# Kernel optimization log

Hardware: AMD Instinct MI355X
Metric: run time of the kernel (lower is better)

## Reference

```python
import jax, jax.numpy as jnp
import numpy as np
from functools import partial

L, B, E, H, NL = 512, 16, 768, 12, 12
D = E // H  # head dim = 64
FF = 4 * E
LN_EPS = 1e-5


def gelu_new(x):
    # HF openai-gpt ACT_FNS['gelu'] (tanh approximation)
    c = np.sqrt(2.0 / np.pi).astype(np.float32)
    return 0.5 * x * (1.0 + jnp.tanh(c * (x + 0.044715 * x * x * x)))


def layer_norm(x, g, b):
    mu = jnp.mean(x, axis=-1, keepdims=True)
    var = jnp.mean(jnp.square(x - mu), axis=-1, keepdims=True)
    return (x - mu) * jax.lax.rsqrt(var + LN_EPS) * g + b


def setup_inputs() -> dict:
    key = jax.random.key(0)
    ks = jax.random.split(key, 8)
    s = 0.02
    x = jax.random.normal(ks[0], (L, B, E), dtype=jnp.float32)
    custom_mask = jnp.ones((B, L), dtype=jnp.float32)
    pos_emb = s * jax.random.normal(ks[1], (L, E), dtype=jnp.float32)
    # stacked per-layer params (leading axis = layer)
    params = {
        'c_attn_w': s * jax.random.normal(ks[2], (NL, E, 3 * E), dtype=jnp.float32),
        'c_attn_b': jnp.zeros((NL, 3 * E), dtype=jnp.float32),
        'attn_proj_w': s * jax.random.normal(ks[3], (NL, E, E), dtype=jnp.float32),
        'attn_proj_b': jnp.zeros((NL, E), dtype=jnp.float32),
        'ln1_g': jnp.ones((NL, E), dtype=jnp.float32),
        'ln1_b': jnp.zeros((NL, E), dtype=jnp.float32),
        'c_fc_w': s * jax.random.normal(ks[4], (NL, E, FF), dtype=jnp.float32),
        'c_fc_b': jnp.zeros((NL, FF), dtype=jnp.float32),
        'mlp_proj_w': s * jax.random.normal(ks[5], (NL, FF, E), dtype=jnp.float32),
        'mlp_proj_b': jnp.zeros((NL, E), dtype=jnp.float32),
        'ln2_g': jnp.ones((NL, E), dtype=jnp.float32),
        'ln2_b': jnp.zeros((NL, E), dtype=jnp.float32),
    }
    return {'x': x, 'custom_mask': custom_mask, 'pos_emb': pos_emb, **params}


def _gpt_forward(x, custom_mask, pos_emb, c_attn_w, c_attn_b, attn_proj_w,
                 attn_proj_b, ln1_g, ln1_b, c_fc_w, c_fc_b, mlp_proj_w,
                 mlp_proj_b, ln2_g, ln2_b):
    Lx, Bx, Ex = x.shape
    h = x.transpose(1, 0, 2) + pos_emb[None, :Lx]  # (B, L, E); dropout = eval identity
    # additive padding mask: (1 - m) * finfo.min, broadcast over heads/queries
    add_mask = (1.0 - custom_mask)[:, None, None, :] * jnp.finfo(jnp.float32).min
    causal = jnp.tril(jnp.ones((Lx, Lx), dtype=jnp.float32))  # bias buffer b

    def block(h, p):
        (caw, cab, apw, apb, g1, b1, fw, fb, pw, pb, g2, b2) = p
        qkv = h @ caw + cab                              # (B, L, 3E)
        q, k, v = jnp.split(qkv, 3, axis=-1)
        q = q.reshape(Bx, Lx, H, D).transpose(0, 2, 1, 3)  # (B, H, L, D)
        k = k.reshape(Bx, Lx, H, D).transpose(0, 2, 1, 3)
        v = v.reshape(Bx, Lx, H, D).transpose(0, 2, 1, 3)
        w = jnp.einsum('bhqd,bhkd->bhqk', q, k) / np.float32(np.sqrt(D))
        w = w * causal + (-10000.0) * (1.0 - causal)     # causal bias masking
        w = w + add_mask
        a = jax.nn.softmax(w, axis=-1)
        o = jnp.einsum('bhqk,bhkd->bhqd', a, v)          # (B, H, L, D)
        o = o.transpose(0, 2, 1, 3).reshape(Bx, Lx, Ex)
        a_out = o @ apw + apb
        n = layer_norm(h + a_out, g1, b1)
        m = gelu_new(n @ fw + fb) @ pw + pb
        h2 = layer_norm(n + m, g2, b2)
        return h2, None

    params = (c_attn_w, c_attn_b, attn_proj_w, attn_proj_b, ln1_g, ln1_b,
              c_fc_w, c_fc_b, mlp_proj_w, mlp_proj_b, ln2_g, ln2_b)
    h, _ = jax.lax.scan(block, h, params)
    return h.transpose(1, 0, 2)  # back to (L, B, E)


def reference(x, custom_mask, pos_emb, c_attn_w, c_attn_b, attn_proj_w,
              attn_proj_b, ln1_g, ln1_b, c_fc_w, c_fc_b, mlp_proj_w,
              mlp_proj_b, ln2_g, ln2_b):
    return _gpt_forward(x, custom_mask, pos_emb, c_attn_w, c_attn_b,
                        attn_proj_w, attn_proj_b, ln1_g, ln1_b, c_fc_w,
                        c_fc_b, mlp_proj_w, mlp_proj_b, ln2_g, ln2_b)
```

## Files before the change

### kernel.cpp

```cpp
#include <hip/hip_runtime.h>
#include <cstdint>
#include <cstddef>


#define LSEQ 512
#define NBATCH 16
#define EDIM 768
#define NHEAD 12
#define NLAYER 12

typedef __attribute__((ext_vector_type(8))) short short8;
typedef __attribute__((ext_vector_type(4))) float f32x4;

__device__ __forceinline__ short f2bf(float f) {
  union { float f; unsigned u; } x; x.f = f;
  return (short)((x.u + 0x7FFFu + ((x.u >> 16) & 1u)) >> 16);
}

__device__ __forceinline__ void gload_lds16(const void* g, void* l) {
  __builtin_amdgcn_global_load_lds(
      (__attribute__((address_space(1))) void*)(void*)g,
      (__attribute__((address_space(3))) void*)l, 16, 0, 0);
}

__global__ __launch_bounds__(256) void wt_transpose(const float* __restrict__ W,
                                                    short* __restrict__ Wt,
                                                    int K, int N) {
  __shared__ float tile[32][33];
  const int n0 = blockIdx.x * 32, k0 = blockIdx.y * 32;
  const size_t lo = (size_t)blockIdx.z * K * N;
  const float* Ws = W + lo;
  short* Wd = Wt + lo;
  const int tx = threadIdx.x & 31, ty = threadIdx.x >> 5;
#pragma unroll
  for (int i = 0; i < 4; ++i)
    tile[ty + i * 8][tx] = Ws[(size_t)(k0 + ty + i * 8) * N + n0 + tx];
  __syncthreads();
#pragma unroll
  for (int i = 0; i < 4; ++i)
    Wd[(size_t)(n0 + ty + i * 8) * K + k0 + tx] = f2bf(tile[tx][ty + i * 8]);
}

__global__ __launch_bounds__(256) void embed_k(const float* __restrict__ x,
                                               const float* __restrict__ pos,
                                               float* __restrict__ h,
                                               short* __restrict__ hbf) {
  const int row = blockIdx.x;
  const int b = row >> 9, lp = row & 511;
  const int t = threadIdx.x;
#pragma unroll
  for (int i = 0; i < 3; ++i) {
    const int e = t + i * 256;
    float v = x[(size_t)(lp * 16 + b) * 768 + e] + pos[(size_t)lp * 768 + e];
    h[(size_t)row * 768 + e] = v;
    hbf[(size_t)row * 768 + e] = f2bf(v);
  }
}

__global__ __launch_bounds__(256) void final_k(const float* __restrict__ h,
                                               float* __restrict__ out) {
  const int row = blockIdx.x;
  const int lp = row >> 4, b = row & 15;
  const int t = threadIdx.x;
#pragma unroll
  for (int i = 0; i < 3; ++i) {
    const int e = t + i * 256;
    out[(size_t)row * 768 + e] = h[(size_t)(b * 512 + lp) * 768 + e];
  }
}

__global__ __launch_bounds__(256) void ln_fused(const float* __restrict__ A,
                                                const float* __restrict__ B,
                                                const float* __restrict__ g,
                                                const float* __restrict__ be,
                                                float* __restrict__ outf,
                                                short* __restrict__ outb) {
  const int row = blockIdx.x;
  const int t = threadIdx.x;
  const size_t base = (size_t)row * 768;
  float v[3];
  float s1 = 0.f, s2 = 0.f;
#pragma unroll
  for (int i = 0; i < 3; ++i) {
    const int e = t + i * 256;
    float xv = A[base + e] + B[base + e];
    v[i] = xv; s1 += xv; s2 += xv * xv;
  }
#pragma unroll
  for (int m = 1; m < 64; m <<= 1) {
    s1 += __shfl_xor(s1, m);
    s2 += __shfl_xor(s2, m);
  }
  __shared__ float r1[4], r2[4];
  const int w = t >> 6, l = t & 63;
  if (l == 0) { r1[w] = s1; r2[w] = s2; }
  __syncthreads();
  s1 = r1[0] + r1[1] + r1[2] + r1[3];
  s2 = r2[0] + r2[1] + r2[2] + r2[3];
  const float mu = s1 * (1.f / 768.f);
  const float var = s2 * (1.f / 768.f) - mu * mu;
  const float rs = rsqrtf(var + 1e-5f);
#pragma unroll
  for (int i = 0; i < 3; ++i) {
    const int e = t + i * 256;
    float o = (v[i] - mu) * rs * g[e] + be[e];
    outf[base + e] = o;
    outb[base + e] = f2bf(o);
  }
}

template <int TN, int EPI>
__global__ __launch_bounds__(256) void gemm_bt(const short* __restrict__ A,
                                               const short* __restrict__ Bt,
                                               const float* __restrict__ bias,
                                               void* __restrict__ C,
                                               int N, int K) {
  constexpr int BK = 64;
  __shared__ alignas(16) short Alds[128 * BK];
  __shared__ alignas(16) short Blds[TN * BK];
  const int t = threadIdx.x;
  const int w = t >> 6, l = t & 63;
  constexpr int WR = (TN == 128) ? 2 : 4;
  constexpr int WC = (TN == 128) ? 2 : 1;
  constexpr int WM = 128 / WR;
  constexpr int MI = WM / 16;
  constexpr int NI = (TN / WC) / 16;
  const int wr = (WC == 2) ? (w >> 1) : w;
  const int wc = (WC == 2) ? (w & 1) : 0;
  const int l15 = l & 15, lhi = l >> 4;
  const int rowA0 = blockIdx.x * 128;
  const int rowB0 = blockIdx.y * TN;
  f32x4 acc[MI][NI];
#pragma unroll
  for (int mi = 0; mi < MI; ++mi)
#pragma unroll
    for (int ni = 0; ni < NI; ++ni) acc[mi][ni] = (f32x4){0.f, 0.f, 0.f, 0.f};

  const int srl = l >> 3;
  const int ss = l & 7;

  for (int kt = 0; kt < K; kt += BK) {
#pragma unroll
    for (int i = 0; i < 4; ++i) {
      const int r = i * 32 + w * 8 + srl;
      gload_lds16(A + (size_t)(rowA0 + r) * K + kt + ((ss ^ (r & 7)) << 3),
                  &Alds[i * 2048 + w * 512]);
    }
#pragma unroll
    for (int i = 0; i < TN / 32; ++i) {
      const int r = i * 32 + w * 8 + srl;
      gload_lds16(Bt + (size_t)(rowB0 + r) * K + kt + ((ss ^ (r & 7)) << 3),
                  &Blds[i * 2048 + w * 512]);
    }
    __syncthreads();
    short8 af[MI][2], bfr[NI][2];
#pragma unroll
    for (int mi = 0; mi < MI; ++mi) {
      const int r = wr * WM + mi * 16 + l15;
#pragma unroll
      for (int kc = 0; kc < 2; ++kc)
        af[mi][kc] = *(const short8*)
            &Alds[r * 64 + ((((kc << 2) | lhi) ^ (r & 7)) << 3)];
    }
#pragma unroll
    for (int ni = 0; ni < NI; ++ni) {
      const int r = wc * 64 + ni * 16 + l15;
#pragma unroll
      for (int kc = 0; kc < 2; ++kc)
        bfr[ni][kc] = *(const short8*)
            &Blds[r * 64 + ((((kc << 2) | lhi) ^ (r & 7)) << 3)];
    }
#pragma unroll
    for (int mi = 0; mi < MI; ++mi)
#pragma unroll
      for (int ni = 0; ni < NI; ++ni)
#pragma unroll
        for (int kc = 0; kc < 2; ++kc)
          acc[mi][ni] = __builtin_amdgcn_mfma_f32_16x16x32_bf16(
              af[mi][kc], bfr[ni][kc], acc[mi][ni], 0, 0, 0);
    __syncthreads();
  }

  float bv[NI];
#pragma unroll
  for (int ni = 0; ni < NI; ++ni) bv[ni] = bias[rowB0 + wc * 64 + ni * 16 + l15];
#pragma unroll
  for (int mi = 0; mi < MI; ++mi) {
#pragma unroll
    for (int ni = 0; ni < NI; ++ni) {
      const int col = rowB0 + wc * 64 + ni * 16 + l15;
#pragma unroll
      for (int i = 0; i < 4; ++i) {
        const int row = rowA0 + wr * WM + mi * 16 + lhi * 4 + i;
        float v = acc[mi][ni][i] + bv[ni];
        if constexpr (EPI == 0) {
          ((float*)C)[(size_t)row * N + col] = v;
        } else if constexpr (EPI == 1) {
          ((short*)C)[(size_t)row * N + col] = f2bf(v);
        } else {
          float z = 0.7978845608028654f * (v + 0.044715f * v * v * v);
          float th = 1.0f - 2.0f / (__expf(2.0f * z) + 1.0f);
          ((short*)C)[(size_t)row * N + col] = f2bf(0.5f * v * (1.0f + th));
        }
      }
    }
  }
}

__global__ __launch_bounds__(256) void attn_k(const short* __restrict__ qkv,
                                              const float* __restrict__ mask,
                                              short* __restrict__ o) {
  const int qb = blockIdx.x;
  const int hh = blockIdx.y;
  const int b = blockIdx.z;
  const int t = threadIdx.x, w = t >> 6, l = t & 63;
  const int l15 = l & 15, lhi = l >> 4;
  __shared__ alignas(16) short Klds[64 * 64];
  __shared__ alignas(16) short Vlds[64 * 64];
  __shared__ alignas(16) short Plds[4][16 * 72];

  short8 qa[2];
  {
    const size_t base =
        (size_t)(b * LSEQ + qb * 64 + w * 16 + l15) * 2304 + hh * 64;
    qa[0] = *(const short8*)&qkv[base + lhi * 8];
    qa[1] = *(const short8*)&qkv[base + 32 + lhi * 8];
  }
  float mrow[4] = {-1e30f, -1e30f, -1e30f, -1e30f};
  float lrow[4] = {0.f, 0.f, 0.f, 0.f};
  const f32x4 zero4 = {0.f, 0.f, 0.f, 0.f};
  f32x4 oacc[4];
#pragma unroll
  for (int nt = 0; nt < 4; ++nt) oacc[nt] = zero4;

  const int nkt = qb + 1;
  for (int kt = 0; kt < nkt; ++kt) {
    __syncthreads();
    {
      const int kr = t >> 2, cc = (t & 3) * 16;
      const size_t grow = (size_t)(b * LSEQ + kt * 64 + kr) * 2304 + hh * 64;
      short8 k0 = *(const short8*)&qkv[grow + 768 + cc];
      short8 k1 = *(const short8*)&qkv[grow + 768 + cc + 8];
      short8 v0 = *(const short8*)&qkv[grow + 1536 + cc];
      short8 v1 = *(const short8*)&qkv[grow + 1536 + cc + 8];
      const int sw = (kr & 7) << 4;
      *(short8*)((char*)Klds + ((kr * 128 + cc * 2) ^ sw)) = k0;
      *(short8*)((char*)Klds + ((kr * 128 + cc * 2 + 16) ^ sw)) = k1;
#pragma unroll
      for (int e = 0; e < 8; ++e) {
        const int n0 = cc + e, n1 = cc + 8 + e;
        ((short*)Vlds)[((n0 * 128 + kr * 2) ^ ((n0 & 7) << 4)) >> 1] = v0[e];
        ((short*)Vlds)[((n1 * 128 + kr * 2) ^ ((n1 & 7) << 4)) >> 1] = v1[e];
      }
    }
    __syncthreads();

    f32x4 s[4];
#pragma unroll
    for (int jt = 0; jt < 4; ++jt) {
      f32x4 z = zero4;
#pragma unroll
      for (int kc = 0; kc < 2; ++kc) {
        const int rowk = jt * 16 + l15;
        short8 kb = *(const short8*)((char*)Klds +
                     ((rowk * 128 + kc * 64 + lhi * 16) ^ ((rowk & 7) << 4)));
        z = __builtin_amdgcn_mfma_f32_16x16x32_bf16(qa[kc], kb, z, 0, 0, 0);
      }
      s[jt] = z;
    }

    float addm[4];
#pragma unroll
    for (int jt = 0; jt < 4; ++jt)
      addm[jt] = (1.0f - mask[b * LSEQ + kt * 64 + jt * 16 + l15]) *
                 -3.402823466e38f;
#pragma unroll
    for (int jt = 0; jt < 4; ++jt) {
      const int colg = kt * 64 + jt * 16 + l15;
#pragma unroll
      for (int i = 0; i < 4; ++i) {
        const int rowg = qb * 64 + w * 16 + lhi * 4 + i;
        float sv = s[jt][i] * 0.125f;
        if (colg > rowg) sv = -10000.0f;
        s[jt][i] = sv + addm[jt];
      }
    }

    float mnew[4], sc[4];
#pragma unroll
    for (int i = 0; i < 4; ++i) {
      float tm = fmaxf(fmaxf(s[0][i], s[1][i]), fmaxf(s[2][i], s[3][i]));
#pragma unroll
      for (int mm = 1; mm < 16; mm <<= 1) tm = fmaxf(tm, __shfl_xor(tm, mm));
      mnew[i] = fmaxf(mrow[i], tm);
      sc[i] = __expf(mrow[i] - mnew[i]);
      mrow[i] = mnew[i];
    }
#pragma unroll
    for (int i = 0; i < 4; ++i) {
      float ts = 0.f;
#pragma unroll
      for (int jt = 0; jt < 4; ++jt) {
        float p = __expf(s[jt][i] - mnew[i]);
        s[jt][i] = p;
        ts += p;
      }
#pragma unroll
      for (int mm = 1; mm < 16; mm <<= 1) ts += __shfl_xor(ts, mm);
      lrow[i] = lrow[i] * sc[i] + ts;
      oacc[0][i] *= sc[i]; oacc[1][i] *= sc[i];
      oacc[2][i] *= sc[i]; oacc[3][i] *= sc[i];
    }

    short* Pw = &Plds[w][0];
#pragma unroll
    for (int jt = 0; jt < 4; ++jt)
#pragma unroll
      for (int i = 0; i < 4; ++i)
        Pw[(lhi * 4 + i) * 72 + jt * 16 + l15] = f2bf(s[jt][i]);
    __syncthreads();
    short8 pa[2];
#pragma unroll
    for (int kc = 0; kc < 2; ++kc)
      pa[kc] = *(const short8*)&Pw[l15 * 72 + kc * 32 + lhi * 8];

#pragma unroll
    for (int nt = 0; nt < 4; ++nt) {
#pragma unroll
      for (int kc = 0; kc < 2; ++kc) {
        const int rown = nt * 16 + l15;
        short8 vb = *(const short8*)((char*)Vlds +
                     ((rown * 128 + kc * 64 + lhi * 16) ^ ((rown & 7) << 4)));
        oacc[nt] = __builtin_amdgcn_mfma_f32_16x16x32_bf16(pa[kc], vb,
                                                           oacc[nt], 0, 0, 0);
      }
    }
  }

#pragma unroll
  for (int i = 0; i < 4; ++i) {
    const size_t row = (size_t)(b * LSEQ + qb * 64 + w * 16 + lhi * 4 + i);
    const float inv = 1.0f / lrow[i];
#pragma unroll
    for (int nt = 0; nt < 4; ++nt)
      o[row * 768 + hh * 64 + nt * 16 + l15] = f2bf(oacc[nt][i] * inv);
  }
}

extern "C" void kernel_launch(void* const* d_in, const int* in_sizes, int n_in,
                              void* d_out, int out_size, void* d_ws,
                              size_t ws_size, hipStream_t stream) {
  const float* x    = (const float*)d_in[0];
  const float* mask = (const float*)d_in[1];
  const float* pos  = (const float*)d_in[2];
  const float* caw  = (const float*)d_in[3];
  const float* cab  = (const float*)d_in[4];
  const float* apw  = (const float*)d_in[5];
  const float* apb  = (const float*)d_in[6];
  const float* g1   = (const float*)d_in[7];
  const float* b1   = (const float*)d_in[8];
  const float* fw   = (const float*)d_in[9];
  const float* fb   = (const float*)d_in[10];
  const float* pw   = (const float*)d_in[11];
  const float* pb   = (const float*)d_in[12];
  const float* g2   = (const float*)d_in[13];
  const float* b2   = (const float*)d_in[14];

  char* ws = (char*)d_ws;
  size_t off = 0;
  auto alloc = [&](size_t bytes) {
    size_t o = off;
    off += (bytes + 255) & ~(size_t)255;
    return o;
  };
  float* h    = (float*)(ws + alloc(8192ull * 768 * 4));
  short* hbf  = (short*)(ws + alloc(8192ull * 768 * 2));
  float* nrm  = (float*)(ws + alloc(8192ull * 768 * 4));
  short* nbf  = (short*)(ws + alloc(8192ull * 768 * 2));
  short* qkvb = (short*)(ws + alloc(8192ull * 2304 * 2));
  short* obf  = (short*)(ws + alloc(8192ull * 768 * 2));
  float* aout = (float*)(ws + alloc(8192ull * 768 * 4));
  short* gbf  = (short*)(ws + alloc(8192ull * 3072 * 2));
  short* wt_attn = (short*)(ws + alloc(12ull * 768 * 2304 * 2));
  short* wt_proj = (short*)(ws + alloc(12ull * 768 * 768 * 2));
  short* wt_fc   = (short*)(ws + alloc(12ull * 768 * 3072 * 2));
  short* wt_mlp  = (short*)(ws + alloc(12ull * 3072 * 768 * 2));
  (void)ws_size; (void)in_sizes; (void)n_in; (void)out_size;

  wt_transpose<<<dim3(2304 / 32, 768 / 32, 12), 256, 0, stream>>>(caw, wt_attn, 768, 2304);
  wt_transpose<<<dim3(768 / 32, 768 / 32, 12), 256, 0, stream>>>(apw, wt_proj, 768, 768);
  wt_transpose<<<dim3(3072 / 32, 768 / 32, 12), 256, 0, stream>>>(fw, wt_fc, 768, 3072);
  wt_transpose<<<dim3(768 / 32, 3072 / 32, 12), 256, 0, stream>>>(pw, wt_mlp, 3072, 768);

  embed_k<<<8192, 256, 0, stream>>>(x, pos, h, hbf);

  for (int L = 0; L < 12; ++L) {
    gemm_bt<128, 1><<<dim3(64, 18), 256, 0, stream>>>(
        hbf, wt_attn + (size_t)L * 2304 * 768, cab + (size_t)L * 2304, qkvb, 2304, 768);
    attn_k<<<dim3(8, 12, 16), 256, 0, stream>>>(qkvb, mask, obf);
    gemm_bt<64, 0><<<dim3(64, 12), 256, 0, stream>>>(
        obf, wt_proj + (size_t)L * 768 * 768, apb + (size_t)L * 768, aout, 768, 768);
    ln_fused<<<8192, 256, 0, stream>>>(h, aout, g1 + (size_t)L * 768,
                                       b1 + (size_t)L * 768, nrm, nbf);
    gemm_bt<128, 2><<<dim3(64, 24), 256, 0, stream>>>(
        nbf, wt_fc + (size_t)L * 768 * 3072, fb + (size_t)L * 3072, gbf, 3072, 768);
    gemm_bt<64, 0><<<dim3(64, 12), 256, 0, stream>>>(
        gbf, wt_mlp + (size_t)L * 3072 * 768, pb + (size_t)L * 768, aout, 768, 3072);
    ln_fused<<<8192, 256, 0, stream>>>(nrm, aout, g2 + (size_t)L * 768,
                                       b2 + (size_t)L * 768, h, hbf);
  }

  final_k<<<8192, 256, 0, stream>>>(h, (float*)d_out);
}
```

Before: 3.372 ms.

## Add 256x256 double-buffered GEMM for QKV/FC, bf16 residual outputs, wave-per-row LN

Adds a new 512-thread GEMM with 256x256 tiles, XOR-swizzled LDS, double-buffered async global-to-LDS loads, interleaved prefetch and raised wave priority around MFMA. It replaces the older GEMM for the QKV and FC projections to get more data reuse per block. The output projections now write bf16 instead of fp32, which halves the traffic into LayerNorm. LayerNorm is rewritten as one wave per row with vectorized loads and no LDS reduction. GELU is rewritten as a sigmoid form using a fast reciprocal. Storing the residual branch in bf16 costs some precision, and the 256-wide tiles launch only 288 or 384 blocks, so the grid may not fill the GPU evenly.

```diff
diff --git a/kernel.cpp b/kernel.cpp
--- a/kernel.cpp
+++ b/kernel.cpp
@@ -10,11 +10,16 @@
 #define NLAYER 12
 
 typedef __attribute__((ext_vector_type(8))) short short8;
+typedef __attribute__((ext_vector_type(4))) short short4v;
 typedef __attribute__((ext_vector_type(4))) float f32x4;
 
 __device__ __forceinline__ short f2bf(float f) {
   union { float f; unsigned u; } x; x.f = f;
   return (short)((x.u + 0x7FFFu + ((x.u >> 16) & 1u)) >> 16);
+}
+__device__ __forceinline__ float bf2f(short s) {
+  union { unsigned u; float f; } x; x.u = ((unsigned)(unsigned short)s) << 16;
+  return x.f;
 }
 
 __device__ __forceinline__ void gload_lds16(const void* g, void* l) {
@@ -70,42 +75,169 @@
 }
 
 __global__ __launch_bounds__(256) void ln_fused(const float* __restrict__ A,
-                                                const float* __restrict__ B,
+                                                const short* __restrict__ B,
                                                 const float* __restrict__ g,
                                                 const float* __restrict__ be,
                                                 float* __restrict__ outf,
                                                 short* __restrict__ outb) {
-  const int row = blockIdx.x;
-  const int t = threadIdx.x;
+  const int row = blockIdx.x * 4 + (threadIdx.x >> 6);
+  const int l = threadIdx.x & 63;
   const size_t base = (size_t)row * 768;
-  float v[3];
+  float v[12];
   float s1 = 0.f, s2 = 0.f;
 #pragma unroll
-  for (int i = 0; i < 3; ++i) {
-    const int e = t + i * 256;
-    float xv = A[base + e] + B[base + e];
-    v[i] = xv; s1 += xv; s2 += xv * xv;
+  for (int j = 0; j < 3; ++j) {
+    const int e = j * 256 + l * 4;
+    f32x4 a = *(const f32x4*)&A[base + e];
+    short4v b = *(const short4v*)&B[base + e];
+#pragma unroll
+    for (int q = 0; q < 4; ++q) {
+      float x = a[q] + bf2f(b[q]);
+      v[j * 4 + q] = x; s1 += x; s2 += x * x;
+    }
   }
 #pragma unroll
   for (int m = 1; m < 64; m <<= 1) {
     s1 += __shfl_xor(s1, m);
     s2 += __shfl_xor(s2, m);
   }
-  __shared__ float r1[4], r2[4];
+  const float mu = s1 * (1.f / 768.f);
+  const float rs = rsqrtf(s2 * (1.f / 768.f) - mu * mu + 1e-5f);
+#pragma unroll
+  for (int j = 0; j < 3; ++j) {
+    const int e = j * 256 + l * 4;
+    f32x4 gv = *(const f32x4*)&g[e];
+    f32x4 bv = *(const f32x4*)&be[e];
+    f32x4 of; short4v ob;
+#pragma unroll
+    for (int q = 0; q < 4; ++q) {
+      float o = (v[j * 4 + q] - mu) * rs * gv[q] + bv[q];
+      of[q] = o; ob[q] = f2bf(o);
+    }
+    *(f32x4*)&outf[base + e] = of;
+    *(short4v*)&outb[base + e] = ob;
+  }
+}
+
+template <int EPI>
+__global__ __launch_bounds__(512, 1) void gemm8(const short* __restrict__ A,
+                                                const short* __restrict__ Bt,
+                                                const float* __restrict__ bias,
+                                                short* __restrict__ C,
+                                                int N, int K) {
+  __shared__ alignas(16) short Ab[2][256 * 64];
+  __shared__ alignas(16) short Bb[2][256 * 64];
+  const int t = threadIdx.x;
   const int w = t >> 6, l = t & 63;
-  if (l == 0) { r1[w] = s1; r2[w] = s2; }
-  __syncthreads();
-  s1 = r1[0] + r1[1] + r1[2] + r1[3];
-  s2 = r2[0] + r2[1] + r2[2] + r2[3];
-  const float mu = s1 * (1.f / 768.f);
-  const float var = s2 * (1.f / 768.f) - mu * mu;
-  const float rs = rsqrtf(var + 1e-5f);
-#pragma unroll
-  for (int i = 0; i < 3; ++i) {
-    const int e = t + i * 256;
-    float o = (v[i] - mu) * rs * g[e] + be[e];
-    outf[base + e] = o;
-    outb[base + e] = f2bf(o);
+  const int wr = w >> 2, wc = w & 3;
+  const int l15 = l & 15, lhi = l >> 4;
+  const int rowA0 = blockIdx.x * 256;
+  const int rowB0 = blockIdx.y * 256;
+  const int nk = K >> 6;
+  const int sr = l >> 3, sl = l & 7;
+
+  f32x4 acc[8][4];
+#pragma unroll
+  for (int a = 0; a < 8; ++a)
+#pragma unroll
+    for (int b = 0; b < 4; ++b) acc[a][b] = (f32x4){0.f, 0.f, 0.f, 0.f};
+
+  auto stageA = [&](int buf, int tile, int half) {
+#pragma unroll
+    for (int i = 0; i < 2; ++i) {
+      const int rb = half * 128 + (i * 8 + w) * 8;
+      const int r = rb + sr;
+      gload_lds16(A + (size_t)(rowA0 + r) * K + tile * 64 + ((sl ^ (r & 7)) << 3),
+                  &Ab[buf][rb * 64]);
+    }
+  };
+  auto stageB = [&](int buf, int tile, int half) {
+#pragma unroll
+    for (int i = 0; i < 2; ++i) {
+      const int rb = half * 128 + (i * 8 + w) * 8;
+      const int r = rb + sr;
+      gload_lds16(Bt + (size_t)(rowB0 + r) * K + tile * 64 + ((sl ^ (r & 7)) << 3),
+                  &Bb[buf][rb * 64]);
+    }
+  };
+
+  stageA(0, 0, 0); stageA(0, 0, 1);
+  stageB(0, 0, 0); stageB(0, 0, 1);
+  if (nk > 1) { stageB(1, 1, 0); stageB(1, 1, 1); }
+  asm volatile("s_waitcnt vmcnt(4)" ::: "memory");
+  __builtin_amdgcn_s_barrier();
+
+  short8 bfr[4][2];
+  for (int U = 0; U < nk; ++U) {
+    const int cur = U & 1, nxt = cur ^ 1;
+#pragma unroll
+    for (int p = 0; p < 4; ++p) {
+      short8 af[2][2];
+#pragma unroll
+      for (int rt = 0; rt < 2; ++rt)
+#pragma unroll
+        for (int kc = 0; kc < 2; ++kc) {
+          const int r = wr * 128 + p * 32 + rt * 16 + l15;
+          af[rt][kc] = *(const short8*)
+              &Ab[cur][r * 64 + ((((kc << 2) | lhi) ^ (r & 7)) << 3)];
+        }
+      if (p == 0) {
+#pragma unroll
+        for (int ct = 0; ct < 4; ++ct)
+#pragma unroll
+          for (int kc = 0; kc < 2; ++kc) {
+            const int r = wc * 64 + ct * 16 + l15;
+            bfr[ct][kc] = *(const short8*)
+                &Bb[cur][r * 64 + ((((kc << 2) | lhi) ^ (r & 7)) << 3)];
+          }
+      }
+      if (p == 0 && U + 1 < nk) stageA(nxt, U + 1, 0);
+      if (p == 1 && U + 1 < nk) stageA(nxt, U + 1, 1);
+      if (p == 2 && U + 2 < nk) stageB(cur, U + 2, 0);
+      if (p == 3 && U + 2 < nk) stageB(cur, U + 2, 1);
+      if (p == 3) {
+        if (U + 2 < nk) asm volatile("s_waitcnt vmcnt(4)" ::: "memory");
+        else            asm volatile("s_waitcnt vmcnt(0)" ::: "memory");
+      }
+      __builtin_amdgcn_s_barrier();
+      asm volatile("s_waitcnt lgkmcnt(0)" ::: "memory");
+      __builtin_amdgcn_sched_barrier(0);
+      __builtin_amdgcn_s_setprio(1);
+#pragma unroll
+      for (int rt = 0; rt < 2; ++rt)
+#pragma unroll
+        for (int ct = 0; ct < 4; ++ct)
+#pragma unroll
+          for (int kc = 0; kc < 2; ++kc)
+            acc[p * 2 + rt][ct] = __builtin_amdgcn_mfma_f32_16x16x32_bf16(
+                af[rt][kc], bfr[ct][kc], acc[p * 2 + rt][ct], 0, 0, 0);
+      __builtin_amdgcn_s_setprio(0);
+      __builtin_amdgcn_s_barrier();
+    }
+  }
+
+  float bv[4];
+#pragma unroll
+  for (int ct = 0; ct < 4; ++ct) bv[ct] = bias[rowB0 + wc * 64 + ct * 16 + l15];
+#pragma unroll
+  for (int rt = 0; rt < 8; ++rt) {
+#pragma unroll
+    for (int ct = 0; ct < 4; ++ct) {
+      const int col = rowB0 + wc * 64 + ct * 16 + l15;
+#pragma unroll
+      for (int i = 0; i < 4; ++i) {
+        const int row = rowA0 + wr * 128 + rt * 16 + lhi * 4 + i;
+        float v = acc[rt][ct][i] + bv[ct];
+        if constexpr (EPI == 1) {
+          C[(size_t)row * N + col] = f2bf(v);
+        } else {
+          float pz = v * fmaf(0.044715f, v * v, 1.0f);
+          float e = __expf(-1.5957691216057308f * pz);
+          float r = __builtin_amdgcn_rcpf(1.0f + e);
+          C[(size_t)row * N + col] = f2bf(v * r);
+        }
+      }
+    }
   }
 }
 
@@ -195,12 +327,8 @@
         float v = acc[mi][ni][i] + bv[ni];
         if constexpr (EPI == 0) {
           ((float*)C)[(size_t)row * N + col] = v;
-        } else if constexpr (EPI == 1) {
+        } else {
           ((short*)C)[(size_t)row * N + col] = f2bf(v);
-        } else {
-          float z = 0.7978845608028654f * (v + 0.044715f * v * v * v);
-          float th = 1.0f - 2.0f / (__expf(2.0f * z) + 1.0f);
-          ((short*)C)[(size_t)row * N + col] = f2bf(0.5f * v * (1.0f + th));
         }
       }
     }
@@ -379,7 +507,7 @@
   short* nbf  = (short*)(ws + alloc(8192ull * 768 * 2));
   short* qkvb = (short*)(ws + alloc(8192ull * 2304 * 2));
   short* obf  = (short*)(ws + alloc(8192ull * 768 * 2));
-  float* aout = (float*)(ws + alloc(8192ull * 768 * 4));
+  short* aout = (short*)(ws + alloc(8192ull * 768 * 2));
   short* gbf  = (short*)(ws + alloc(8192ull * 3072 * 2));
   short* wt_attn = (short*)(ws + alloc(12ull * 768 * 2304 * 2));
   short* wt_proj = (short*)(ws + alloc(12ull * 768 * 768 * 2));
@@ -395,18 +523,18 @@
   embed_k<<<8192, 256, 0, stream>>>(x, pos, h, hbf);
 
   for (int L = 0; L < 12; ++L) {
-    gemm_bt<128, 1><<<dim3(64, 18), 256, 0, stream>>>(
+    gemm8<1><<<dim3(32, 9), 512, 0, stream>>>(
         hbf, wt_attn + (size_t)L * 2304 * 768, cab + (size_t)L * 2304, qkvb, 2304, 768);
     attn_k<<<dim3(8, 12, 16), 256, 0, stream>>>(qkvb, mask, obf);
-    gemm_bt<64, 0><<<dim3(64, 12), 256, 0, stream>>>(
+    gemm_bt<64, 1><<<dim3(64, 12), 256, 0, stream>>>(
         obf, wt_proj + (size_t)L * 768 * 768, apb + (size_t)L * 768, aout, 768, 768);
-    ln_fused<<<8192, 256, 0, stream>>>(h, aout, g1 + (size_t)L * 768,
+    ln_fused<<<2048, 256, 0, stream>>>(h, aout, g1 + (size_t)L * 768,
                                        b1 + (size_t)L * 768, nrm, nbf);
-    gemm_bt<128, 2><<<dim3(64, 24), 256, 0, stream>>>(
+    gemm8<2><<<dim3(32, 12), 512, 0, stream>>>(
         nbf, wt_fc + (size_t)L * 768 * 3072, fb + (size_t)L * 3072, gbf, 3072, 768);
-    gemm_bt<64, 0><<<dim3(64, 12), 256, 0, stream>>>(
+    gemm_bt<64, 1><<<dim3(64, 12), 256, 0, stream>>>(
         gbf, wt_mlp + (size_t)L * 3072 * 768, pb + (size_t)L * 768, aout, 768, 3072);
-    ln_fused<<<8192, 256, 0, stream>>>(nrm, aout, g2 + (size_t)L * 768,
+    ln_fused<<<2048, 256, 0, stream>>>(nrm, aout, g2 + (size_t)L * 768,
                                        b2 + (size_t)L * 768, h, hbf);
   }
 
```

After: 3.550 ms. 5.3% more time.
